# Optimization experiments

Hardware: AMD Instinct MI355X
Metric: run time of the kernel (lower is better)

## Reference

```python
import jax, jax.numpy as jnp
import numpy as np

B, S, D, H = 2, 2048, 1024, 16
DK = D // H

def setup_inputs() -> dict:
    key = jax.random.key(0)
    ks = jax.random.split(key, 12)
    s = 1.0 / np.sqrt(D)
    return {
        "q": jax.random.normal(ks[0], (B, S, D), jnp.float32),
        "k": jax.random.normal(ks[1], (B, S, D), jnp.float32),
        "v": jax.random.normal(ks[2], (B, S, D), jnp.float32),
        "mask": jnp.ones((1, 1, S, S), jnp.int32),
        "Wq": jax.random.normal(ks[3], (D, D), jnp.float32) * s,
        "bq": jnp.zeros((D,), jnp.float32),
        "Wk": jax.random.normal(ks[4], (D, D), jnp.float32) * s,
        "bk": jnp.zeros((D,), jnp.float32),
        "Wv": jax.random.normal(ks[5], (D, D), jnp.float32) * s,
        "bv": jnp.zeros((D,), jnp.float32),
        "Wo": jax.random.normal(ks[6], (D, D), jnp.float32) * s,
        "bo": jnp.zeros((D,), jnp.float32),
    }

def reference(q, k, v, mask, Wq, bq, Wk, bk, Wv, bv, Wo, bo):
    # projections (torch Linear: x @ W^T + b)
    Q = q @ Wq.T + bq
    K = k @ Wk.T + bk
    V = v @ Wv.T + bv
    # split heads: [B,S,D] -> [B,H,S,DK]
    def split(x):
        return x.reshape(B, S, H, DK).transpose(0, 2, 1, 3)
    Qh, Kh, Vh = split(Q), split(K), split(V)
    scores = jnp.einsum('bhqd,bhkd->bhqk', Qh, Kh) / jnp.sqrt(jnp.float32(DK))
    scores = jnp.where(mask == 0, jnp.float32(-1e9), scores)
    attn = jax.nn.softmax(scores, axis=-1)  # dropout p=0.0 -> identity
    x = jnp.einsum('bhqk,bhkd->bhqd', attn, Vh)
    x = x.transpose(0, 2, 1, 3).reshape(B, S, D)
    return x @ Wo.T + bo
```

## Files before the change

### kernel.cpp

```cpp
#include <hip/hip_runtime.h>
#include <hip/hip_bf16.h>
#include <stdint.h>

#define B_    2
#define S_    2048
#define D_    1024
#define H_    16
#define NTOK  (B_ * S_)

typedef __attribute__((ext_vector_type(8))) short bf16x8;
typedef __attribute__((ext_vector_type(4))) float f32x4;
typedef __attribute__((ext_vector_type(2))) float float2v;
typedef __attribute__((ext_vector_type(2))) __bf16 bfv2;

static __device__ __forceinline__ unsigned int pkbf(float a, float b) {
    float2v fv = {a, b};
    bfv2 r = __builtin_convertvector(fv, bfv2);
    unsigned int u;
    __builtin_memcpy(&u, &r, 4);
    return u;
}

using g_cu32 = __attribute__((address_space(1))) const unsigned int;
using l_u32  = __attribute__((address_space(3))) unsigned int;
static __device__ __forceinline__ void gld16(const void* g, void* l) {
    __builtin_amdgcn_global_load_lds((g_cu32*)g, (l_u32*)l, 16, 0, 0);
}

template<int N> static __device__ __forceinline__ void wait_vm() {
    if constexpr (N == 0)      asm volatile("s_waitcnt vmcnt(0)" ::: "memory");
    else if constexpr (N == 2) asm volatile("s_waitcnt vmcnt(2)" ::: "memory");
    else if constexpr (N == 3) asm volatile("s_waitcnt vmcnt(3)" ::: "memory");
    else if constexpr (N == 4) asm volatile("s_waitcnt vmcnt(4)" ::: "memory");
}

#define QN ((size_t)NTOK * D_)
#define WN ((size_t)D_ * D_)

struct SwapT { static constexpr bool value = true; };
struct NoSwapT { static constexpr bool value = false; };

__global__ __launch_bounds__(256) void prep_kernel(
    const float* __restrict__ q, const float* __restrict__ k, const float* __restrict__ v,
    const float* __restrict__ Wq, const float* __restrict__ Wk,
    const float* __restrict__ Wv, const float* __restrict__ Wo,
    const int* __restrict__ mask,
    unsigned short* __restrict__ qb, unsigned short* __restrict__ kb,
    unsigned short* __restrict__ vb, unsigned short* __restrict__ wqb,
    unsigned short* __restrict__ wkb, unsigned short* __restrict__ wvb,
    unsigned short* __restrict__ wob, int* __restrict__ flags) {
    __shared__ int anyz;
    if (blockIdx.x < 4096) {
        size_t i = ((size_t)blockIdx.x * 256 + threadIdx.x) * 16;
        const float* s; unsigned short* d; size_t off;
        if (i < QN)          { s = q; d = qb; off = i; }
        else if (i < 2 * QN) { s = k; d = kb; off = i - QN; }
        else if (i < 3 * QN) { s = v; d = vb; off = i - 2 * QN; }
        else {
            size_t j = i - 3 * QN;
            int wi = (int)(j >> 20);
            s = (wi == 0) ? Wq : (wi == 1) ? Wk : (wi == 2) ? Wv : Wo;
            d = (wi == 0) ? wqb : (wi == 1) ? wkb : (wi == 2) ? wvb : wob;
            off = j & (WN - 1);
        }
        float4 a0 = *(const float4*)(s + off);
        float4 a1 = *(const float4*)(s + off + 4);
        float4 a2 = *(const float4*)(s + off + 8);
        float4 a3 = *(const float4*)(s + off + 12);
        uint4 p0, p1;
        p0.x = pkbf(a0.x, a0.y); p0.y = pkbf(a0.z, a0.w);
        p0.z = pkbf(a1.x, a1.y); p0.w = pkbf(a1.z, a1.w);
        p1.x = pkbf(a2.x, a2.y); p1.y = pkbf(a2.z, a2.w);
        p1.z = pkbf(a3.x, a3.y); p1.w = pkbf(a3.z, a3.w);
        *(uint4*)(d + off)     = p0;
        *(uint4*)(d + off + 8) = p1;
    } else {
        if (threadIdx.x == 0) anyz = 0;
        __syncthreads();
        int bid2 = blockIdx.x - 4096;
        const int qt = bid2 >> 5, kt = bid2 & 31;
        int az = 0;
        for (int i = threadIdx.x; i < 64 * 64; i += 256) {
            int r = i >> 6, c = i & 63;
            az |= (mask[(size_t)(qt * 64 + r) * S_ + kt * 64 + c] == 0) ? 1 : 0;
        }
        if (az) atomicOr(&anyz, 1);
        __syncthreads();
        if (threadIdx.x == 0) flags[qt * 32 + kt] = anyz;
    }
}

struct GemmArgs {
    const unsigned short* A[3];
    const unsigned short* W[3];
    const float* bias[3];
    void* C[3];
    int mode[3];
    float scale[3];
};

template<int BMT>
__global__ __launch_bounds__(256, 3) void gemm_async(GemmArgs ga) {
    constexpr int AG = BMT / 16;
    constexpr int MI = BMT / 32;
    constexpr int NK = D_ / 32;
    constexpr int LOADS = (BMT == 128) ? 4 : 3;
    const int z = blockIdx.z;
    const unsigned short* __restrict__ A = ga.A[z];
    const unsigned short* __restrict__ W = ga.W[z];
    const float* __restrict__ bias = ga.bias[z];
    void* C = ga.C[z];
    const int mode = ga.mode[z];
    const float scl = ga.scale[z];

    __shared__ unsigned short As[3][AG * 512];
    __shared__ unsigned short Bs[3][8 * 512];

    const int t    = threadIdx.x;
    const int lane = t & 63;
    const int w    = t >> 6;
    const int fr   = lane & 15;
    const int kq   = lane >> 4;
    const int wrow = w >> 1, wcol = w & 1;
    const int m0 = blockIdx.x * BMT, n0 = blockIdx.y * 128;

    const int sc = lane >> 4;
    const int sr = lane & 15;

    const unsigned short* ga0;
    const unsigned short* ga1 = nullptr;
    int la0Off, la1Off = 0;
    if constexpr (BMT == 128) {
        ga0 = A + (size_t)(m0 + (2 * w) * 16 + sr) * D_ + sc * 8;
        ga1 = ga0 + 16 * D_;
        la0Off = (2 * w) * 512;
        la1Off = (2 * w + 1) * 512;
    } else {
        ga0 = A + (size_t)(m0 + w * 16 + sr) * D_ + sc * 8;
        la0Off = w * 512;
    }
    const unsigned short* gw0 = W + (size_t)(n0 + (2 * w) * 16 + sr) * D_ + sc * 8;
    const unsigned short* gw1 = gw0 + 16 * D_;
    const int lw0Off = (2 * w) * 512;
    const int lw1Off = (2 * w + 1) * 512;

    int aOff[MI], bOff[4];
#pragma unroll
    for (int mi = 0; mi < MI; ++mi) aOff[mi] = (wrow * MI + mi) * 512 + (kq * 16 + fr) * 8;
#pragma unroll
    for (int ni = 0; ni < 4; ++ni) bOff[ni] = (wcol * 4 + ni) * 512 + (kq * 16 + fr) * 8;

    f32x4 acc[MI][4];
#pragma unroll
    for (int i = 0; i < MI; ++i)
#pragma unroll
        for (int j = 0; j < 4; ++j) acc[i][j] = (f32x4)0.0f;

    auto stage = [&](int buf) {
        gld16(ga0, &As[buf][la0Off]);
        if constexpr (BMT == 128) gld16(ga1, &As[buf][la1Off]);
        gld16(gw0, &Bs[buf][lw0Off]);
        gld16(gw1, &Bs[buf][lw1Off]);
        ga0 += 32; gw0 += 32; gw1 += 32;
        if constexpr (BMT == 128) ga1 += 32;
    };

    auto kloop = [&](auto swc) {
        constexpr bool SW = decltype(swc)::value;
        auto mma_step = [&](int cur) {
            const unsigned short* Ab = As[cur];
            const unsigned short* Bb = Bs[cur];
            bf16x8 af[MI], bfr[4];
#pragma unroll
            for (int mi = 0; mi < MI; ++mi) af[mi] = *(const bf16x8*)&Ab[aOff[mi]];
#pragma unroll
            for (int ni = 0; ni < 4; ++ni) bfr[ni] = *(const bf16x8*)&Bb[bOff[ni]];
#pragma unroll
            for (int mi = 0; mi < MI; ++mi)
#pragma unroll
                for (int ni = 0; ni < 4; ++ni) {
                    if constexpr (SW)
                        acc[mi][ni] = __builtin_amdgcn_mfma_f32_16x16x32_bf16(
                            bfr[ni], af[mi], acc[mi][ni], 0, 0, 0);
                    else
                        acc[mi][ni] = __builtin_amdgcn_mfma_f32_16x16x32_bf16(
                            af[mi], bfr[ni], acc[mi][ni], 0, 0, 0);
                }
        };

        stage(0);
        stage(1);
        int cur = 0;
        for (int k0 = 0; k0 < NK - 1; ++k0) {
            __builtin_amdgcn_sched_barrier(0);
            wait_vm<LOADS>();
            __builtin_amdgcn_s_barrier();
            __builtin_amdgcn_sched_barrier(0);
            if (k0 + 2 < NK) {
                int pf = (cur >= 1) ? cur - 1 : cur + 2;
                stage(pf);
            }
            mma_step(cur);
            cur = (cur < 2) ? cur + 1 : 0;
        }
        __builtin_amdgcn_sched_barrier(0);
        wait_vm<0>();
        __builtin_amdgcn_s_barrier();
        __builtin_amdgcn_sched_barrier(0);
        mma_step(cur);
    };
    if (mode == 2) kloop(NoSwapT{}); else kloop(SwapT{});

    if (mode == 2) {
        unsigned short* Co = (unsigned short*)C;
#pragma unroll
        for (int ni = 0; ni < 4; ++ni) {
            int col = n0 + wcol * 64 + ni * 16 + fr;
            float bv = bias[col];
            int hh = col >> 6, d = col & 63;
#pragma unroll
            for (int mi = 0; mi < MI; ++mi) {
                int tok = m0 + wrow * (BMT / 2) + mi * 16 + kq * 4;
                int bb = tok >> 11, sbase = tok & (S_ - 1);
                uint2 pk;
                pk.x = pkbf((acc[mi][ni][0] + bv) * scl, (acc[mi][ni][1] + bv) * scl);
                pk.y = pkbf((acc[mi][ni][2] + bv) * scl, (acc[mi][ni][3] + bv) * scl);
                *(uint2*)(Co + ((size_t)((bb * H_ + hh) * 64 + d)) * S_ + sbase) = pk;
            }
        }
    } else if (mode == 0) {
        float* Co = (float*)C;
#pragma unroll
        for (int ni = 0; ni < 4; ++ni) {
            int nb = n0 + wcol * 64 + ni * 16 + kq * 4;
            float4 b4 = *(const float4*)&bias[nb];
#pragma unroll
            for (int mi = 0; mi < MI; ++mi) {
                int m = m0 + wrow * (BMT / 2) + mi * 16 + fr;
                float4 o4;
                o4.x = (acc[mi][ni][0] + b4.x) * scl;
                o4.y = (acc[mi][ni][1] + b4.y) * scl;
                o4.z = (acc[mi][ni][2] + b4.z) * scl;
                o4.w = (acc[mi][ni][3] + b4.w) * scl;
                *(float4*)(Co + (size_t)m * D_ + nb) = o4;
            }
        }
    } else {
        unsigned short* Co = (unsigned short*)C;
#pragma unroll
        for (int ni = 0; ni < 4; ++ni) {
            int nb = n0 + wcol * 64 + ni * 16 + kq * 4;
            float4 b4 = *(const float4*)&bias[nb];
#pragma unroll
            for (int mi = 0; mi < MI; ++mi) {
                int m = m0 + wrow * (BMT / 2) + mi * 16 + fr;
                uint2 pk;
                pk.x = pkbf((acc[mi][ni][0] + b4.x) * scl, (acc[mi][ni][1] + b4.y) * scl);
                pk.y = pkbf((acc[mi][ni][2] + b4.z) * scl, (acc[mi][ni][3] + b4.w) * scl);
                *(uint2*)(Co + (size_t)m * D_ + nb) = pk;
            }
        }
    }
}

__global__ __launch_bounds__(512, 4) void flash4(
    const unsigned short* __restrict__ Qb, const unsigned short* __restrict__ Kb,
    const unsigned short* __restrict__ Vtg, const int* __restrict__ mask,
    const int* __restrict__ flags, unsigned short* __restrict__ Xb) {
    __shared__ unsigned short Ks[3][4096];
    __shared__ unsigned short Vs[3][4096];
    __shared__ unsigned short Ps[8192];

    const int t    = threadIdx.x;
    const int lane = t & 63;
    const int w    = t >> 6;
    const int fr   = lane & 15;
    const int kq   = lane >> 4;
    const int bid = blockIdx.x;
    const int swb = ((bid & 7) << 6) | (bid >> 3);
    const int qt = swb & 15, hd = (swb >> 4) & 15, b = swb >> 8;
    const int q0 = qt * 128;
    const int swz = fr & 7;

    const unsigned short* qrow_p = Qb + (size_t)(b * S_ + q0 + w * 16 + fr) * D_ + hd * 64;
    bf16x8 qf[2];
    qf[0] = *(const bf16x8*)(qrow_p + kq * 8);
    qf[1] = *(const bf16x8*)(qrow_p + 32 + kq * 8);

    int fl = (lane < 32) ? flags[(qt * 2 + (w >> 2)) * 32 + lane] : 0;
    unsigned int fmask = (unsigned int)__ballot(fl != 0);

    const unsigned short* kptr =
        Kb + (size_t)(b * S_ + (w >> 1) * 16 + fr) * D_ + hd * 64 + (w & 1) * 32 + kq * 8;
    const unsigned short* vptr =
        Vtg + ((size_t)((b * H_ + hd) * 64 + (w >> 1) * 16 + fr)) * S_ + (w & 1) * 32 + kq * 8;

    gld16(kptr, (char*)&Ks[0][0] + w * 1024);
    gld16(vptr, (char*)&Vs[0][0] + w * 1024);
    gld16(kptr + (size_t)64 * D_, (char*)&Ks[1][0] + w * 1024);
    gld16(vptr + 64,              (char*)&Vs[1][0] + w * 1024);
    const unsigned short* kpf = kptr + (size_t)128 * D_;
    const unsigned short* vpf = vptr + 128;

    unsigned short* pswr[4];
#pragma unroll
    for (int mi = 0; mi < 4; ++mi) {
        int chunk = mi * 2 + (kq >> 1);
        pswr[mi] = &Ps[(w * 16 + fr) * 64 + ((chunk ^ swz) << 3) + ((kq & 1) << 2)];
    }
    const unsigned short* psrd[2];
#pragma unroll
    for (int kk = 0; kk < 2; ++kk) {
        int c = kk * 4 + kq;
        psrd[kk] = &Ps[(w * 16 + fr) * 64 + ((c ^ swz) << 3)];
    }

    const f32x4 zf = (f32x4)0.0f;
    f32x4 o[4];
#pragma unroll
    for (int i = 0; i < 4; ++i) o[i] = zf;
    float2v l2 = {0.0f, 0.0f};

    auto attn_step = [&](int cur, int kt) {
        f32x4 st[4];
#pragma unroll
        for (int mi = 0; mi < 4; ++mi) {
            bf16x8 a = *(const bf16x8*)&Ks[cur][mi * 1024 + (kq * 16 + fr) * 8];
            st[mi] = __builtin_amdgcn_mfma_f32_16x16x32_bf16(a, qf[0], zf, 0, 0, 0);
        }
#pragma unroll
        for (int mi = 0; mi < 4; ++mi) {
            bf16x8 a = *(const bf16x8*)&Ks[cur][mi * 1024 + ((4 + kq) * 16 + fr) * 8];
            st[mi] = __builtin_amdgcn_mfma_f32_16x16x32_bf16(a, qf[1], st[mi], 0, 0, 0);
        }

        if ((fmask >> kt) & 1u) {
#pragma unroll
            for (int mi = 0; mi < 4; ++mi) {
                int4 mv = *(const int4*)&mask[(size_t)(q0 + w * 16 + fr) * S_ + kt * 64 + mi * 16 + kq * 4];
                if (mv.x == 0) st[mi][0] = -3e8f;
                if (mv.y == 0) st[mi][1] = -3e8f;
                if (mv.z == 0) st[mi][2] = -3e8f;
                if (mv.w == 0) st[mi][3] = -3e8f;
            }
        }

#pragma unroll
        for (int mi = 0; mi < 4; ++mi) {
            float e0 = __builtin_amdgcn_exp2f(st[mi][0]);
            float e1 = __builtin_amdgcn_exp2f(st[mi][1]);
            float e2 = __builtin_amdgcn_exp2f(st[mi][2]);
            float e3 = __builtin_amdgcn_exp2f(st[mi][3]);
            l2 += (float2v){e0, e1} + (float2v){e2, e3};
            uint2 pk;
            pk.x = pkbf(e0, e1);
            pk.y = pkbf(e2, e3);
            *(uint2*)pswr[mi] = pk;
        }

#pragma unroll
        for (int kk = 0; kk < 2; ++kk) {
            bf16x8 pb = *(const bf16x8*)psrd[kk];
#pragma unroll
            for (int mi = 0; mi < 4; ++mi) {
                bf16x8 a = *(const bf16x8*)&Vs[cur][mi * 1024 + ((kk * 4 + kq) * 16 + fr) * 8];
                o[mi] = __builtin_amdgcn_mfma_f32_16x16x32_bf16(a, pb, o[mi], 0, 0, 0);
            }
        }
    };

    int cur = 0;
    for (int kt = 0; kt < 31; ++kt) {
        __builtin_amdgcn_sched_barrier(0);
        wait_vm<2>();
        __builtin_amdgcn_s_barrier();
        __builtin_amdgcn_sched_barrier(0);
        if (kt < 30) {
            int pf = (cur >= 1) ? cur - 1 : cur + 2;
            gld16(kpf, (char*)&Ks[pf][0] + w * 1024);
            gld16(vpf, (char*)&Vs[pf][0] + w * 1024);
            kpf += (size_t)64 * D_;
            vpf += 64;
        }
        attn_step(cur, kt);
        cur = (cur < 2) ? cur + 1 : 0;
    }
    __builtin_amdgcn_sched_barrier(0);
    wait_vm<0>();
    __builtin_amdgcn_s_barrier();
    __builtin_amdgcn_sched_barrier(0);
    attn_step(cur, 31);

    float l_i = l2.x + l2.y;
    l_i += __shfl_xor(l_i, 16, 64);
    l_i += __shfl_xor(l_i, 32, 64);
    float rl = 1.0f / l_i;

#pragma unroll
    for (int mi = 0; mi < 4; ++mi) {
        uint2 pk;
        pk.x = pkbf(o[mi][0] * rl, o[mi][1] * rl);
        pk.y = pkbf(o[mi][2] * rl, o[mi][3] * rl);
        *(uint2*)(Xb + (size_t)(b * S_ + q0 + w * 16 + fr) * D_ + hd * 64 + mi * 16 + kq * 4) = pk;
    }
}

extern "C" void kernel_launch(void* const* d_in, const int* in_sizes, int n_in,
                              void* d_out, int out_size, void* d_ws, size_t ws_size,
                              hipStream_t stream) {
    const float* q    = (const float*)d_in[0];
    const float* k    = (const float*)d_in[1];
    const float* v    = (const float*)d_in[2];
    const int*   mask = (const int*)d_in[3];
    const float* Wq   = (const float*)d_in[4];
    const float* bq   = (const float*)d_in[5];
    const float* Wk   = (const float*)d_in[6];
    const float* bk   = (const float*)d_in[7];
    const float* Wv   = (const float*)d_in[8];
    const float* bv   = (const float*)d_in[9];
    const float* Wo   = (const float*)d_in[10];
    const float* bo   = (const float*)d_in[11];
    float* out = (float*)d_out;

    unsigned short* qb  = (unsigned short*)d_ws;
    unsigned short* kb  = qb + QN;
    unsigned short* vb  = kb + QN;
    unsigned short* Qf  = vb + QN;
    unsigned short* Kf  = Qf + QN;
    unsigned short* Vt  = Kf + QN;
    unsigned short* wqb = Vt + QN;
    unsigned short* wkb = wqb + WN;
    unsigned short* wvb = wkb + WN;
    unsigned short* wob = wvb + WN;
    int* flags = (int*)(wob + WN);

    const float SC = 0.18033688011112042f;

    prep_kernel<<<5120, 256, 0, stream>>>(q, k, v, Wq, Wk, Wv, Wo, mask,
                                          qb, kb, vb, wqb, wkb, wvb, wob, flags);

    GemmArgs g1;
    g1.A[0] = qb;  g1.W[0] = wqb; g1.bias[0] = bq; g1.C[0] = Qf; g1.mode[0] = 1; g1.scale[0] = SC;
    g1.A[1] = kb;  g1.W[1] = wkb; g1.bias[1] = bk; g1.C[1] = Kf; g1.mode[1] = 1; g1.scale[1] = 1.0f;
    g1.A[2] = vb;  g1.W[2] = wvb; g1.bias[2] = bv; g1.C[2] = Vt; g1.mode[2] = 2; g1.scale[2] = 1.0f;
    gemm_async<128><<<dim3(NTOK / 128, D_ / 128, 3), 256, 0, stream>>>(g1);

    flash4<<<dim3((S_ / 128) * H_ * B_, 1, 1), 512, 0, stream>>>(Qf, Kf, Vt, mask, flags, Qf);

    GemmArgs g2;
    g2.A[0] = Qf; g2.W[0] = wob; g2.bias[0] = bo; g2.C[0] = out; g2.mode[0] = 0; g2.scale[0] = 1.0f;
    g2.A[1] = g2.A[2] = nullptr; g2.W[1] = g2.W[2] = nullptr;
    g2.bias[1] = g2.bias[2] = nullptr; g2.C[1] = g2.C[2] = nullptr;
    g2.mode[1] = g2.mode[2] = 0; g2.scale[1] = g2.scale[2] = 1.0f;
    gemm_async<64><<<dim3(NTOK / 64, D_ / 128, 1), 256, 0, stream>>>(g2);
}
```

Measured before the change: 261.1 us.

## Rework flash attention to 32x32x16 MFMA with key-split warps sharing P

Switches the attention kernel from 16x16x32 to 32x32x16 bf16 MFMA tiles. Each warp now owns 32 query rows and half of the 64-key tile, and writes its exp'd scores to a shared P buffer. A block barrier then lets every warp multiply the full P row slice against its share of V. The row sums from the two key halves are combined through LDS at the end. The larger MFMA shape cuts instruction count and LDS fragment reads, but it adds an extra block-wide barrier per key tile and cross-warp dependencies through P.

Result: no change. 261.5 us (+0.1%).

```diff
diff --git a/kernel.cpp b/kernel.cpp
--- a/kernel.cpp
+++ b/kernel.cpp
@@ -10,6 +10,7 @@
 
 typedef __attribute__((ext_vector_type(8))) short bf16x8;
 typedef __attribute__((ext_vector_type(4))) float f32x4;
+typedef __attribute__((ext_vector_type(16))) float f32x16;
 typedef __attribute__((ext_vector_type(2))) float float2v;
 typedef __attribute__((ext_vector_type(2))) __bf16 bfv2;
 
@@ -274,98 +275,105 @@
     const int t    = threadIdx.x;
     const int lane = t & 63;
     const int w    = t >> 6;
-    const int fr   = lane & 15;
-    const int kq   = lane >> 4;
+    const int r31  = lane & 31;
+    const int hi   = lane >> 5;
+    const int qc   = w & 3;
+    const int kg   = w >> 2;
     const int bid = blockIdx.x;
     const int swb = ((bid & 7) << 6) | (bid >> 3);
     const int qt = swb & 15, hd = (swb >> 4) & 15, b = swb >> 8;
     const int q0 = qt * 128;
-    const int swz = fr & 7;
-
-    const unsigned short* qrow_p = Qb + (size_t)(b * S_ + q0 + w * 16 + fr) * D_ + hd * 64;
-    bf16x8 qf[2];
-    qf[0] = *(const bf16x8*)(qrow_p + kq * 8);
-    qf[1] = *(const bf16x8*)(qrow_p + 32 + kq * 8);
-
-    int fl = (lane < 32) ? flags[(qt * 2 + (w >> 2)) * 32 + lane] : 0;
+    const int qloc = qc * 32 + r31;
+    const int qglob = q0 + qloc;
+
+    const unsigned short* qrow_p = Qb + (size_t)(b * S_ + qglob) * D_ + hd * 64;
+    bf16x8 qfr[4];
+#pragma unroll
+    for (int tt = 0; tt < 4; ++tt)
+        qfr[tt] = *(const bf16x8*)(qrow_p + tt * 16 + hi * 8);
+
+    int fl = (lane < 32) ? flags[(qt * 2 + (qc >> 1)) * 32 + lane] : 0;
     unsigned int fmask = (unsigned int)__ballot(fl != 0);
 
     const unsigned short* kptr =
-        Kb + (size_t)(b * S_ + (w >> 1) * 16 + fr) * D_ + hd * 64 + (w & 1) * 32 + kq * 8;
+        Kb + (size_t)(b * S_ + kg * 32 + r31) * D_ + hd * 64 + qc * 16 + hi * 8;
     const unsigned short* vptr =
-        Vtg + ((size_t)((b * H_ + hd) * 64 + (w >> 1) * 16 + fr)) * S_ + (w & 1) * 32 + kq * 8;
-
-    gld16(kptr, (char*)&Ks[0][0] + w * 1024);
-    gld16(vptr, (char*)&Vs[0][0] + w * 1024);
-    gld16(kptr + (size_t)64 * D_, (char*)&Ks[1][0] + w * 1024);
-    gld16(vptr + 64,              (char*)&Vs[1][0] + w * 1024);
+        Vtg + ((size_t)((b * H_ + hd) * 64 + kg * 32 + r31)) * S_ + qc * 16 + hi * 8;
+
+    auto stageKV = [&](int buf, const unsigned short* kp, const unsigned short* vp) {
+        gld16(kp, (char*)&Ks[buf][0] + w * 1024);
+        gld16(vp, (char*)&Vs[buf][0] + w * 1024);
+    };
+
+    stageKV(0, kptr, vptr);
+    stageKV(1, kptr + (size_t)64 * D_, vptr + 64);
     const unsigned short* kpf = kptr + (size_t)128 * D_;
     const unsigned short* vpf = vptr + 128;
 
-    unsigned short* pswr[4];
-#pragma unroll
-    for (int mi = 0; mi < 4; ++mi) {
-        int chunk = mi * 2 + (kq >> 1);
-        pswr[mi] = &Ps[(w * 16 + fr) * 64 + ((chunk ^ swz) << 3) + ((kq & 1) << 2)];
-    }
-    const unsigned short* psrd[2];
-#pragma unroll
-    for (int kk = 0; kk < 2; ++kk) {
-        int c = kk * 4 + kq;
-        psrd[kk] = &Ps[(w * 16 + fr) * 64 + ((c ^ swz) << 3)];
-    }
-
-    const f32x4 zf = (f32x4)0.0f;
-    f32x4 o[4];
-#pragma unroll
-    for (int i = 0; i < 4; ++i) o[i] = zf;
+    const int qx = (qloc & 7) << 4;
+    int psw[4], psr[4];
+#pragma unroll
+    for (int t2 = 0; t2 < 4; ++t2)
+        psw[t2] = (qloc << 7) + ((kg * 64 + hi * 8 + t2 * 16) ^ qx);
+#pragma unroll
+    for (int c = 0; c < 4; ++c)
+        psr[c] = (qloc << 7) + ((c * 32 + hi * 16) ^ qx);
+
+    const f32x16 zf16 = (f32x16)0.0f;
+    f32x16 o = zf16;
     float2v l2 = {0.0f, 0.0f};
 
     auto attn_step = [&](int cur, int kt) {
-        f32x4 st[4];
-#pragma unroll
-        for (int mi = 0; mi < 4; ++mi) {
-            bf16x8 a = *(const bf16x8*)&Ks[cur][mi * 1024 + (kq * 16 + fr) * 8];
-            st[mi] = __builtin_amdgcn_mfma_f32_16x16x32_bf16(a, qf[0], zf, 0, 0, 0);
-        }
-#pragma unroll
-        for (int mi = 0; mi < 4; ++mi) {
-            bf16x8 a = *(const bf16x8*)&Ks[cur][mi * 1024 + ((4 + kq) * 16 + fr) * 8];
-            st[mi] = __builtin_amdgcn_mfma_f32_16x16x32_bf16(a, qf[1], st[mi], 0, 0, 0);
+        const char* ksb = (const char*)&Ks[cur][0];
+        const char* vsb = (const char*)&Vs[cur][0];
+        const int lb = lane * 16;
+
+        f32x16 st;
+        {
+            bf16x8 kf = *(const bf16x8*)(ksb + ((kg * 4 + 0) << 10) + lb);
+            st = __builtin_amdgcn_mfma_f32_32x32x16_bf16(kf, qfr[0], zf16, 0, 0, 0);
+        }
+#pragma unroll
+        for (int tt = 1; tt < 4; ++tt) {
+            bf16x8 kf = *(const bf16x8*)(ksb + ((kg * 4 + tt) << 10) + lb);
+            st = __builtin_amdgcn_mfma_f32_32x32x16_bf16(kf, qfr[tt], st, 0, 0, 0);
         }
 
         if ((fmask >> kt) & 1u) {
 #pragma unroll
-            for (int mi = 0; mi < 4; ++mi) {
-                int4 mv = *(const int4*)&mask[(size_t)(q0 + w * 16 + fr) * S_ + kt * 64 + mi * 16 + kq * 4];
-                if (mv.x == 0) st[mi][0] = -3e8f;
-                if (mv.y == 0) st[mi][1] = -3e8f;
-                if (mv.z == 0) st[mi][2] = -3e8f;
-                if (mv.w == 0) st[mi][3] = -3e8f;
+            for (int t2 = 0; t2 < 4; ++t2) {
+                int4 mv = *(const int4*)&mask[(size_t)qglob * S_ + kt * 64 +
+                                              kg * 32 + t2 * 8 + hi * 4];
+                if (mv.x == 0) st[4 * t2 + 0] = -3e8f;
+                if (mv.y == 0) st[4 * t2 + 1] = -3e8f;
+                if (mv.z == 0) st[4 * t2 + 2] = -3e8f;
+                if (mv.w == 0) st[4 * t2 + 3] = -3e8f;
             }
         }
 
 #pragma unroll
-        for (int mi = 0; mi < 4; ++mi) {
-            float e0 = __builtin_amdgcn_exp2f(st[mi][0]);
-            float e1 = __builtin_amdgcn_exp2f(st[mi][1]);
-            float e2 = __builtin_amdgcn_exp2f(st[mi][2]);
-            float e3 = __builtin_amdgcn_exp2f(st[mi][3]);
+        for (int t2 = 0; t2 < 4; ++t2) {
+            float e0 = __builtin_amdgcn_exp2f(st[4 * t2 + 0]);
+            float e1 = __builtin_amdgcn_exp2f(st[4 * t2 + 1]);
+            float e2 = __builtin_amdgcn_exp2f(st[4 * t2 + 2]);
+            float e3 = __builtin_amdgcn_exp2f(st[4 * t2 + 3]);
             l2 += (float2v){e0, e1} + (float2v){e2, e3};
             uint2 pk;
             pk.x = pkbf(e0, e1);
             pk.y = pkbf(e2, e3);
-            *(uint2*)pswr[mi] = pk;
-        }
-
-#pragma unroll
-        for (int kk = 0; kk < 2; ++kk) {
-            bf16x8 pb = *(const bf16x8*)psrd[kk];
-#pragma unroll
-            for (int mi = 0; mi < 4; ++mi) {
-                bf16x8 a = *(const bf16x8*)&Vs[cur][mi * 1024 + ((kk * 4 + kq) * 16 + fr) * 8];
-                o[mi] = __builtin_amdgcn_mfma_f32_16x16x32_bf16(a, pb, o[mi], 0, 0, 0);
-            }
+            *(uint2*)((char*)Ps + psw[t2]) = pk;
+        }
+
+        asm volatile("s_waitcnt lgkmcnt(0)" ::: "memory");
+        __builtin_amdgcn_sched_barrier(0);
+        __builtin_amdgcn_s_barrier();
+        __builtin_amdgcn_sched_barrier(0);
+
+#pragma unroll
+        for (int c = 0; c < 4; ++c) {
+            bf16x8 vf = *(const bf16x8*)(vsb + ((kg * 4 + c) << 10) + lb);
+            bf16x8 pb = *(const bf16x8*)((const char*)Ps + psr[c]);
+            o = __builtin_amdgcn_mfma_f32_32x32x16_bf16(vf, pb, o, 0, 0, 0);
         }
     };
 
@@ -377,8 +385,7 @@
         __builtin_amdgcn_sched_barrier(0);
         if (kt < 30) {
             int pf = (cur >= 1) ? cur - 1 : cur + 2;
-            gld16(kpf, (char*)&Ks[pf][0] + w * 1024);
-            gld16(vpf, (char*)&Vs[pf][0] + w * 1024);
+            stageKV(pf, kpf, vpf);
             kpf += (size_t)64 * D_;
             vpf += 64;
         }
@@ -391,17 +398,21 @@
     __builtin_amdgcn_sched_barrier(0);
     attn_step(cur, 31);
 
-    float l_i = l2.x + l2.y;
-    l_i += __shfl_xor(l_i, 16, 64);
-    l_i += __shfl_xor(l_i, 32, 64);
-    float rl = 1.0f / l_i;
-
-#pragma unroll
-    for (int mi = 0; mi < 4; ++mi) {
+    float l_loc = l2.x + l2.y;
+    l_loc += __shfl_xor(l_loc, 32, 64);
+    __syncthreads();
+    float* Lf = (float*)Ps;
+    Lf[qloc * 2 + kg] = l_loc;
+    __syncthreads();
+    float rl = 1.0f / (Lf[qloc * 2] + Lf[qloc * 2 + 1]);
+
+    unsigned short* xrow = Xb + (size_t)(b * S_ + qglob) * D_ + hd * 64;
+#pragma unroll
+    for (int t2 = 0; t2 < 4; ++t2) {
         uint2 pk;
-        pk.x = pkbf(o[mi][0] * rl, o[mi][1] * rl);
-        pk.y = pkbf(o[mi][2] * rl, o[mi][3] * rl);
-        *(uint2*)(Xb + (size_t)(b * S_ + q0 + w * 16 + fr) * D_ + hd * 64 + mi * 16 + kq * 4) = pk;
+        pk.x = pkbf(o[4 * t2 + 0] * rl, o[4 * t2 + 1] * rl);
+        pk.y = pkbf(o[4 * t2 + 2] * rl, o[4 * t2 + 3] * rl);
+        *(uint2*)(xrow + kg * 32 + t2 * 8 + hi * 4) = pk;
     }
 }
 
```
